# Kernel tuning notes

Hardware: AMD Instinct MI355X
Metric: run time of the kernel (lower is better)

## Reference

```python
import jax, jax.numpy as jnp
import numpy as np

DZ, DB, DS, DX, BATCH, T = 128, 32, 32, 64, 64, 4096


def setup_inputs() -> dict:
    # AW initialized as in PLRNN.init_AW: eye + (1/dz^2) M M^T, spectral norm 1
    rng = np.random.default_rng(0)
    M = rng.standard_normal((DZ, DZ)).astype(np.float32)
    A = np.eye(DZ, dtype=np.float32) + (M @ M.T) / (DZ * DZ)
    A = A / np.max(np.abs(np.linalg.eigvals(A)))
    AW = jnp.asarray(0.95 * A, dtype=jnp.float32)  # 0.95 margin keeps long rollout stable

    key = jax.random.key(0)
    ks = jax.random.split(key, 7)
    z0 = jax.random.normal(ks[0], (BATCH, DZ), dtype=jnp.float32)
    inputs = jax.random.normal(ks[1], (T, DS), dtype=jnp.float32)
    h = 0.1 * jax.random.normal(ks[2], (DZ,), dtype=jnp.float32)
    thetas = 2.0 * jax.random.normal(ks[3], (DZ, DB), dtype=jnp.float32) - 1.0
    alphas = 2.0 * jax.random.normal(ks[4], (DB,), dtype=jnp.float32) - 1.0
    clipping = 5.0 * jnp.ones((DZ, DB), dtype=jnp.float32)  # fixed buffer in torch
    C = 0.1 * jax.random.normal(ks[5], (DZ, DS), dtype=jnp.float32)
    B_obs = jax.random.normal(ks[6], (DZ, DX), dtype=jnp.float32)
    return dict(z0=z0, inputs=inputs, AW=AW, h=h, thetas=thetas,
                alphas=alphas, clipping=clipping, C=C, B_obs=B_obs)


def _leaky(x):
    # nn.LeakyReLU(0.18)
    return jnp.where(x >= 0, x, 0.18 * x)


def reference(z0, inputs, AW, h, thetas, alphas, clipping, C, B_obs):
    # split_diag_offdiag: A = diag(AW), W = AW - diag(AW)
    a_diag = jnp.diag(AW)            # (dz,)
    W = AW - jnp.diag(a_diag)        # (dz, dz), zero diagonal

    def step(z, s):
        # z: (B, dz), s: (ds,)
        d = z[:, :, None] - thetas   # (B, dz, db)
        be = (jnp.sum(alphas * _leaky(d), axis=-1)
              - jnp.sum(alphas * _leaky(d + clipping), axis=-1))  # (B, dz)
        z_new = z * a_diag + be @ W.T + h + (C @ s)  # diag matmul == elementwise
        return z_new, z_new

    _, Z = jax.lax.scan(step, z0, inputs)   # (T, B, dz)
    # torch.cat over list of (B, dz) -> (T*B, dz), time-major
    Z = Z.reshape(-1, Z.shape[-1])
    return Z @ B_obs                        # linear_observation: (T*B, dx)
```

## Files before the change

### kernel.cpp

```cpp
#include <hip/hip_runtime.h>
#include <hip/hip_bf16.h>
#include <hip/hip_fp16.h>

#define DZ 128
#define DB 32
#define DSIN 32
#define DX 64
#define NB 64
#define TT 4096

typedef short v8s __attribute__((ext_vector_type(8)));
typedef float v4f __attribute__((ext_vector_type(4)));
typedef _Float16 v2h __attribute__((ext_vector_type(2)));

__device__ __forceinline__ float dpp_xor1(float x) {
  int y = __builtin_amdgcn_mov_dpp(__builtin_bit_cast(int, x), 0xB1, 0xF, 0xF, true);
  return __builtin_bit_cast(float, y);
}
__device__ __forceinline__ float dpp_xor2(float x) {
  int y = __builtin_amdgcn_mov_dpp(__builtin_bit_cast(int, x), 0x4E, 0xF, 0xF, true);
  return __builtin_bit_cast(float, y);
}

__device__ __forceinline__ short f2bf(float f) {
  __hip_bfloat16 h = __float2bfloat16(f);
  return *reinterpret_cast<short*>(&h);
}

__device__ __forceinline__ unsigned cvt_pk_bf16(float lo, float hi) {
  unsigned r;
  asm volatile("v_cvt_pk_bf16_f32 %0, %1, %2" : "=v"(r) : "v"(lo), "v"(hi));
  return r;
}

__device__ __forceinline__ v2h pk2h(float a, float b) {
  return __builtin_bit_cast(v2h, __builtin_amdgcn_cvt_pkrtz(a, b));
}
__device__ __forceinline__ float fdot2(v2h a, v2h b, float c) {
  return __builtin_amdgcn_fdot2(a, b, c, false);
}

__global__ void k_prep(const float* __restrict__ AW, const float* __restrict__ alphas,
                       const float* __restrict__ clip, float* __restrict__ WCd) {
  __shared__ float cd[DZ];
  int j = threadIdx.x;
  float s = 0.f;
  for (int k = 0; k < DB; ++k) s = fmaf(alphas[k], clip[j * DB + k], s);
  cd[j] = s;
  __syncthreads();
  float acc = 0.f;
  for (int jj = 0; jj < DZ; ++jj)
    if (jj != j) acc = fmaf(AW[j * DZ + jj], cd[jj], acc);
  WCd[j] = acc;
}

__global__ void k_u(const float* __restrict__ inp, const float* __restrict__ h,
                    const float* __restrict__ C, const float* __restrict__ WCd,
                    float* __restrict__ UT) {
  int gid = blockIdx.x * blockDim.x + threadIdx.x;
  int i = gid >> 10;
  int t0 = (gid & 1023) * 4;
  float base = h[i] - WCd[i];
  const float4* c4 = (const float4*)(C + i * DSIN);
  float4 cv[8];
#pragma unroll
  for (int s = 0; s < 8; ++s) cv[s] = c4[s];
  float out[4];
#pragma unroll
  for (int tt = 0; tt < 4; ++tt) {
    const float4* i4 = (const float4*)(inp + (size_t)(t0 + tt) * DSIN);
    float u = base;
#pragma unroll
    for (int s = 0; s < 8; ++s) {
      float4 iv = i4[s];
      u = fmaf(cv[s].x, iv.x, u);
      u = fmaf(cv[s].y, iv.y, u);
      u = fmaf(cv[s].z, iv.z, u);
      u = fmaf(cv[s].w, iv.w, u);
    }
    out[tt] = u;
  }
  *(float4*)(UT + (size_t)i * TT + t0) = make_float4(out[0], out[1], out[2], out[3]);
}

__global__ __launch_bounds__(256, 1) void k_scan(
    const float* __restrict__ z0, const float* __restrict__ AW,
    const float* __restrict__ thetas, const float* __restrict__ alphas,
    const float* __restrict__ clip, const float* __restrict__ UT,
    unsigned* __restrict__ Z32) {
  __shared__ __align__(16) unsigned gpk[2][64];
  const int b = blockIdx.x;
  const int tid = threadIdx.x;
  const int p = tid >> 2, s = tid & 3;
  const int i0 = 2 * p, i1 = i0 + 1;
  const int c0 = 32 * s;

  v2h w0[16], w1[16];
#pragma unroll
  for (int j = 0; j < 16; ++j) {
    float2 a0 = *(const float2*)(AW + (size_t)i0 * DZ + c0 + 2 * j);
    float2 a1 = *(const float2*)(AW + (size_t)i1 * DZ + c0 + 2 * j);
    bool dg = (c0 + 2 * j == i0);
    w0[j] = pk2h(dg ? 0.f : a0.x, a0.y);
    w1[j] = pk2h(a1.x, dg ? 0.f : a1.y);
  }
  const float ad0 = AW[(size_t)i0 * DZ + i0], ad1 = AW[(size_t)i1 * DZ + i1];

  v2h th0[4], th1[4], nc0[4], nc1[4], al[4];
#pragma unroll
  for (int m = 0; m < 4; ++m) {
    int k = 8 * s + 2 * m;
    th0[m] = pk2h(thetas[i0 * DB + k], thetas[i0 * DB + k + 1]);
    th1[m] = pk2h(thetas[i1 * DB + k], thetas[i1 * DB + k + 1]);
    nc0[m] = pk2h(-clip[i0 * DB + k], -clip[i0 * DB + k + 1]);
    nc1[m] = pk2h(-clip[i1 * DB + k], -clip[i1 * DB + k + 1]);
    al[m] = pk2h(-0.82f * alphas[k], -0.82f * alphas[k + 1]);
  }

  float zA = z0[b * DZ + i0], zB = z0[b * DZ + i1];
  const float4* upA = (const float4*)(UT + (size_t)i0 * TT);
  const float4* upB = (const float4*)(UT + (size_t)i1 * TT);
  float4 ugA = upA[0], ugB = upB[0];
  unsigned* zp = Z32 + (size_t)b * 64 + p;
  const v2h zero2 = pk2h(0.f, 0.f);

#pragma unroll 1
  for (int tg = 0; tg < TT / 4; ++tg) {
    int tn = (tg + 1 < TT / 4) ? tg + 1 : tg;
    float4 ugAn = upA[tn], ugBn = upB[tn];
    float uA[4] = {ugA.x, ugA.y, ugA.z, ugA.w};
    float uB[4] = {ugB.x, ugB.y, ugB.z, ugB.w};
#pragma unroll
    for (int q = 0; q < 4; ++q) {
      unsigned* gq = gpk[q & 1];
      v2h zA2 = pk2h(zA, zA), zB2 = pk2h(zB, zB);
      float gA0 = 0.f, gA1 = 0.f, gB0 = 0.f, gB1 = 0.f;
#pragma unroll
      for (int m = 0; m < 4; m += 2) {
        v2h dA0 = __builtin_elementwise_min(
            __builtin_elementwise_max(zA2 - th0[m], nc0[m]), zero2);
        v2h dA1 = __builtin_elementwise_min(
            __builtin_elementwise_max(zA2 - th0[m + 1], nc0[m + 1]), zero2);
        v2h dB0 = __builtin_elementwise_min(
            __builtin_elementwise_max(zB2 - th1[m], nc1[m]), zero2);
        v2h dB1 = __builtin_elementwise_min(
            __builtin_elementwise_max(zB2 - th1[m + 1], nc1[m + 1]), zero2);
        gA0 = fdot2(al[m], dA0, gA0);
        gA1 = fdot2(al[m + 1], dA1, gA1);
        gB0 = fdot2(al[m], dB0, gB0);
        gB1 = fdot2(al[m + 1], dB1, gB1);
      }
      float gA = gA0 + gA1;
      gA += dpp_xor1(gA);
      gA += dpp_xor2(gA);
      float gB = gB0 + gB1;
      gB += dpp_xor1(gB);
      gB += dpp_xor2(gB);
      if (s == 0) gq[p] = __builtin_bit_cast(unsigned, pk2h(gA, gB));
      asm volatile("s_waitcnt lgkmcnt(0)\n\ts_barrier" ::: "memory");

      const uint4* g4 = ((const uint4*)gq) + 4 * s;
      float mA0 = 0.f, mA1 = 0.f, mA2 = 0.f, mA3 = 0.f;
      float mB0 = 0.f, mB1 = 0.f, mB2 = 0.f, mB3 = 0.f;
#pragma unroll
      for (int r = 0; r < 4; ++r) {
        uint4 qd = g4[r];
        v2h q0 = __builtin_bit_cast(v2h, qd.x), q1 = __builtin_bit_cast(v2h, qd.y);
        v2h q2 = __builtin_bit_cast(v2h, qd.z), q3 = __builtin_bit_cast(v2h, qd.w);
        mA0 = fdot2(w0[4 * r + 0], q0, mA0);
        mA1 = fdot2(w0[4 * r + 1], q1, mA1);
        mA2 = fdot2(w0[4 * r + 2], q2, mA2);
        mA3 = fdot2(w0[4 * r + 3], q3, mA3);
        mB0 = fdot2(w1[4 * r + 0], q0, mB0);
        mB1 = fdot2(w1[4 * r + 1], q1, mB1);
        mB2 = fdot2(w1[4 * r + 2], q2, mB2);
        mB3 = fdot2(w1[4 * r + 3], q3, mB3);
      }
      float mA = (mA0 + mA1) + (mA2 + mA3);
      mA += dpp_xor1(mA);
      mA += dpp_xor2(mA);
      float mB = (mB0 + mB1) + (mB2 + mB3);
      mB += dpp_xor1(mB);
      mB += dpp_xor2(mB);
      zA = fmaf(zA, ad0, mA + uA[q]);
      zB = fmaf(zB, ad1, mB + uB[q]);
      if (s == 0) zp[(size_t)(tg * 4 + q) * (NB * 64)] = cvt_pk_bf16(zA, zB);
    }
    ugA = ugAn;
    ugB = ugBn;
  }
}

__global__ __launch_bounds__(256) void k_obs(const short* __restrict__ Z,
                                             const float* __restrict__ Bo,
                                             float* __restrict__ out) {
  const int lane = threadIdx.x & 63;
  const int wv = threadIdx.x >> 6;
  const int rl = lane & 15;
  const int g = lane >> 4;

  v8s bfr[4][4];
#pragma unroll
  for (int nt = 0; nt < 4; ++nt) {
#pragma unroll
    for (int ks = 0; ks < 4; ++ks) {
      v8s f;
#pragma unroll
      for (int m = 0; m < 8; ++m) {
        int k = ks * 32 + g * 8 + m;
        f[m] = f2bf(Bo[k * DX + nt * 16 + rl]);
      }
      bfr[nt][ks] = f;
    }
  }

#pragma unroll
  for (int it = 0; it < 4; ++it) {
    const int r0 = blockIdx.x * 256 + it * 64 + wv * 16;
    const short* zrow = Z + (size_t)(r0 + rl) * DZ;
    v8s afr[4];
#pragma unroll
    for (int ks = 0; ks < 4; ++ks)
      afr[ks] = *(const v8s*)(zrow + ks * 32 + g * 8);
    v4f acc[4];
#pragma unroll
    for (int nt = 0; nt < 4; ++nt) acc[nt] = (v4f){0.f, 0.f, 0.f, 0.f};
#pragma unroll
    for (int nt = 0; nt < 4; ++nt) {
#pragma unroll
      for (int ks = 0; ks < 4; ++ks)
        acc[nt] = __builtin_amdgcn_mfma_f32_16x16x32_bf16(afr[ks], bfr[nt][ks], acc[nt], 0, 0, 0);
    }
#pragma unroll
    for (int nt = 0; nt < 4; ++nt) {
#pragma unroll
      for (int q = 0; q < 4; ++q)
        out[(size_t)(r0 + g * 4 + q) * DX + nt * 16 + rl] = acc[nt][q];
    }
  }
}

extern "C" void kernel_launch(void* const* d_in, const int* in_sizes, int n_in,
                              void* d_out, int out_size, void* d_ws, size_t ws_size,
                              hipStream_t stream) {
  const float* z0 = (const float*)d_in[0];
  const float* inp = (const float*)d_in[1];
  const float* AW = (const float*)d_in[2];
  const float* h = (const float*)d_in[3];
  const float* thetas = (const float*)d_in[4];
  const float* alphas = (const float*)d_in[5];
  const float* clip = (const float*)d_in[6];
  const float* C = (const float*)d_in[7];
  const float* Bo = (const float*)d_in[8];
  float* out = (float*)d_out;

  char* ws = (char*)d_ws;
  float* WCd = (float*)ws;
  float* UT = (float*)(ws + 1024);
  short* Z = (short*)(ws + 1024 + (size_t)TT * DZ * 4);

  k_prep<<<1, 128, 0, stream>>>(AW, alphas, clip, WCd);
  k_u<<<(DZ * TT / 4) / 256, 256, 0, stream>>>(inp, h, C, WCd, UT);
  k_scan<<<NB, 256, 0, stream>>>(z0, AW, thetas, alphas, clip, UT, (unsigned*)Z);
  k_obs<<<(TT * NB) / 256, 256, 0, stream>>>(Z, Bo, out);
}
```

Before: 1.635 ms.

## Process two batch rows per scan block to amortize barriers

The scan kernel now handles two batch elements per workgroup, launching NB/2 blocks instead of NB. Both rows share the same register-resident weights, thresholds and input terms, and one barrier per timestep serves both recurrences, which gives extra independent work to hide latency. The cost is twice the per-step arithmetic on each block's critical path and more register use, while only half as many CUs are occupied.

```diff
diff --git a/kernel.cpp b/kernel.cpp
--- a/kernel.cpp
+++ b/kernel.cpp
@@ -88,8 +88,9 @@
     const float* __restrict__ thetas, const float* __restrict__ alphas,
     const float* __restrict__ clip, const float* __restrict__ UT,
     unsigned* __restrict__ Z32) {
-  __shared__ __align__(16) unsigned gpk[2][64];
-  const int b = blockIdx.x;
+  __shared__ __align__(16) unsigned gpk[2][2][64];
+  const int blk = blockIdx.x;
+  const int b0 = 2 * blk, b1 = b0 + 1;
   const int tid = threadIdx.x;
   const int p = tid >> 2, s = tid & 3;
   const int i0 = 2 * p, i1 = i0 + 1;
@@ -117,11 +118,13 @@
     al[m] = pk2h(-0.82f * alphas[k], -0.82f * alphas[k + 1]);
   }
 
-  float zA = z0[b * DZ + i0], zB = z0[b * DZ + i1];
+  float zA0 = z0[b0 * DZ + i0], zB0 = z0[b0 * DZ + i1];
+  float zA1 = z0[b1 * DZ + i0], zB1 = z0[b1 * DZ + i1];
   const float4* upA = (const float4*)(UT + (size_t)i0 * TT);
   const float4* upB = (const float4*)(UT + (size_t)i1 * TT);
   float4 ugA = upA[0], ugB = upB[0];
-  unsigned* zp = Z32 + (size_t)b * 64 + p;
+  unsigned* zp0 = Z32 + (size_t)b0 * 64 + p;
+  unsigned* zp1 = Z32 + (size_t)b1 * 64 + p;
   const v2h zero2 = pk2h(0.f, 0.f);
 
 #pragma unroll 1
@@ -132,59 +135,122 @@
     float uB[4] = {ugB.x, ugB.y, ugB.z, ugB.w};
 #pragma unroll
     for (int q = 0; q < 4; ++q) {
-      unsigned* gq = gpk[q & 1];
-      v2h zA2 = pk2h(zA, zA), zB2 = pk2h(zB, zB);
-      float gA0 = 0.f, gA1 = 0.f, gB0 = 0.f, gB1 = 0.f;
+      unsigned(*gq)[64] = gpk[q & 1];
+      v2h zA20 = pk2h(zA0, zA0), zB20 = pk2h(zB0, zB0);
+      float gA0a = 0.f, gA0b = 0.f, gB0a = 0.f, gB0b = 0.f;
 #pragma unroll
       for (int m = 0; m < 4; m += 2) {
         v2h dA0 = __builtin_elementwise_min(
-            __builtin_elementwise_max(zA2 - th0[m], nc0[m]), zero2);
+            __builtin_elementwise_max(zA20 - th0[m], nc0[m]), zero2);
         v2h dA1 = __builtin_elementwise_min(
-            __builtin_elementwise_max(zA2 - th0[m + 1], nc0[m + 1]), zero2);
+            __builtin_elementwise_max(zA20 - th0[m + 1], nc0[m + 1]), zero2);
         v2h dB0 = __builtin_elementwise_min(
-            __builtin_elementwise_max(zB2 - th1[m], nc1[m]), zero2);
+            __builtin_elementwise_max(zB20 - th1[m], nc1[m]), zero2);
         v2h dB1 = __builtin_elementwise_min(
-            __builtin_elementwise_max(zB2 - th1[m + 1], nc1[m + 1]), zero2);
-        gA0 = fdot2(al[m], dA0, gA0);
-        gA1 = fdot2(al[m + 1], dA1, gA1);
-        gB0 = fdot2(al[m], dB0, gB0);
-        gB1 = fdot2(al[m + 1], dB1, gB1);
-      }
-      float gA = gA0 + gA1;
-      gA += dpp_xor1(gA);
-      gA += dpp_xor2(gA);
-      float gB = gB0 + gB1;
-      gB += dpp_xor1(gB);
-      gB += dpp_xor2(gB);
-      if (s == 0) gq[p] = __builtin_bit_cast(unsigned, pk2h(gA, gB));
+            __builtin_elementwise_max(zB20 - th1[m + 1], nc1[m + 1]), zero2);
+        gA0a = fdot2(al[m], dA0, gA0a);
+        gA0b = fdot2(al[m + 1], dA1, gA0b);
+        gB0a = fdot2(al[m], dB0, gB0a);
+        gB0b = fdot2(al[m + 1], dB1, gB0b);
+      }
+      float gA_0 = gA0a + gA0b;
+      gA_0 += dpp_xor1(gA_0);
+      gA_0 += dpp_xor2(gA_0);
+      float gB_0 = gB0a + gB0b;
+      gB_0 += dpp_xor1(gB_0);
+      gB_0 += dpp_xor2(gB_0);
+      if (s == 0) gq[0][p] = __builtin_bit_cast(unsigned, pk2h(gA_0, gB_0));
+      v2h zA21 = pk2h(zA1, zA1), zB21 = pk2h(zB1, zB1);
+      float gA1a = 0.f, gA1b = 0.f, gB1a = 0.f, gB1b = 0.f;
+#pragma unroll
+      for (int m = 0; m < 4; m += 2) {
+        v2h dA0 = __builtin_elementwise_min(
+            __builtin_elementwise_max(zA21 - th0[m], nc0[m]), zero2);
+        v2h dA1 = __builtin_elementwise_min(
+            __builtin_elementwise_max(zA21 - th0[m + 1], nc0[m + 1]), zero2);
+        v2h dB0 = __builtin_elementwise_min(
+            __builtin_elementwise_max(zB21 - th1[m], nc1[m]), zero2);
+        v2h dB1 = __builtin_elementwise_min(
+            __builtin_elementwise_max(zB21 - th1[m + 1], nc1[m + 1]), zero2);
+        gA1a = fdot2(al[m], dA0, gA1a);
+        gA1b = fdot2(al[m + 1], dA1, gA1b);
+        gB1a = fdot2(al[m], dB0, gB1a);
+        gB1b = fdot2(al[m + 1], dB1, gB1b);
+      }
+      float gA_1 = gA1a + gA1b;
+      gA_1 += dpp_xor1(gA_1);
+      gA_1 += dpp_xor2(gA_1);
+      float gB_1 = gB1a + gB1b;
+      gB_1 += dpp_xor1(gB_1);
+      gB_1 += dpp_xor2(gB_1);
+      if (s == 0) gq[1][p] = __builtin_bit_cast(unsigned, pk2h(gA_1, gB_1));
       asm volatile("s_waitcnt lgkmcnt(0)\n\ts_barrier" ::: "memory");
 
-      const uint4* g4 = ((const uint4*)gq) + 4 * s;
-      float mA0 = 0.f, mA1 = 0.f, mA2 = 0.f, mA3 = 0.f;
-      float mB0 = 0.f, mB1 = 0.f, mB2 = 0.f, mB3 = 0.f;
-#pragma unroll
-      for (int r = 0; r < 4; ++r) {
-        uint4 qd = g4[r];
-        v2h q0 = __builtin_bit_cast(v2h, qd.x), q1 = __builtin_bit_cast(v2h, qd.y);
-        v2h q2 = __builtin_bit_cast(v2h, qd.z), q3 = __builtin_bit_cast(v2h, qd.w);
-        mA0 = fdot2(w0[4 * r + 0], q0, mA0);
-        mA1 = fdot2(w0[4 * r + 1], q1, mA1);
-        mA2 = fdot2(w0[4 * r + 2], q2, mA2);
-        mA3 = fdot2(w0[4 * r + 3], q3, mA3);
-        mB0 = fdot2(w1[4 * r + 0], q0, mB0);
-        mB1 = fdot2(w1[4 * r + 1], q1, mB1);
-        mB2 = fdot2(w1[4 * r + 2], q2, mB2);
-        mB3 = fdot2(w1[4 * r + 3], q3, mB3);
-      }
-      float mA = (mA0 + mA1) + (mA2 + mA3);
-      mA += dpp_xor1(mA);
-      mA += dpp_xor2(mA);
-      float mB = (mB0 + mB1) + (mB2 + mB3);
-      mB += dpp_xor1(mB);
-      mB += dpp_xor2(mB);
-      zA = fmaf(zA, ad0, mA + uA[q]);
-      zB = fmaf(zB, ad1, mB + uB[q]);
-      if (s == 0) zp[(size_t)(tg * 4 + q) * (NB * 64)] = cvt_pk_bf16(zA, zB);
+      const uint4* g40 = ((const uint4*)gq[0]) + 4 * s;
+      const uint4* g41 = ((const uint4*)gq[1]) + 4 * s;
+      uint4 qd0[4], qd1[4];
+#pragma unroll
+      for (int r = 0; r < 4; ++r) qd0[r] = g40[r];
+#pragma unroll
+      for (int r = 0; r < 4; ++r) qd1[r] = g41[r];
+
+      {
+        float mA0 = 0.f, mA1 = 0.f, mA2 = 0.f, mA3 = 0.f;
+        float mB0 = 0.f, mB1 = 0.f, mB2 = 0.f, mB3 = 0.f;
+#pragma unroll
+        for (int r = 0; r < 4; ++r) {
+          uint4 qd = qd0[r];
+          v2h q0 = __builtin_bit_cast(v2h, qd.x), q1 = __builtin_bit_cast(v2h, qd.y);
+          v2h q2 = __builtin_bit_cast(v2h, qd.z), q3 = __builtin_bit_cast(v2h, qd.w);
+          mA0 = fdot2(w0[4 * r + 0], q0, mA0);
+          mA1 = fdot2(w0[4 * r + 1], q1, mA1);
+          mA2 = fdot2(w0[4 * r + 2], q2, mA2);
+          mA3 = fdot2(w0[4 * r + 3], q3, mA3);
+          mB0 = fdot2(w1[4 * r + 0], q0, mB0);
+          mB1 = fdot2(w1[4 * r + 1], q1, mB1);
+          mB2 = fdot2(w1[4 * r + 2], q2, mB2);
+          mB3 = fdot2(w1[4 * r + 3], q3, mB3);
+        }
+        float mA = (mA0 + mA1) + (mA2 + mA3);
+        mA += dpp_xor1(mA);
+        mA += dpp_xor2(mA);
+        float mB = (mB0 + mB1) + (mB2 + mB3);
+        mB += dpp_xor1(mB);
+        mB += dpp_xor2(mB);
+        zA0 = fmaf(zA0, ad0, mA + uA[q]);
+        zB0 = fmaf(zB0, ad1, mB + uB[q]);
+      }
+      {
+        float mA0 = 0.f, mA1 = 0.f, mA2 = 0.f, mA3 = 0.f;
+        float mB0 = 0.f, mB1 = 0.f, mB2 = 0.f, mB3 = 0.f;
+#pragma unroll
+        for (int r = 0; r < 4; ++r) {
+          uint4 qd = qd1[r];
+          v2h q0 = __builtin_bit_cast(v2h, qd.x), q1 = __builtin_bit_cast(v2h, qd.y);
+          v2h q2 = __builtin_bit_cast(v2h, qd.z), q3 = __builtin_bit_cast(v2h, qd.w);
+          mA0 = fdot2(w0[4 * r + 0], q0, mA0);
+          mA1 = fdot2(w0[4 * r + 1], q1, mA1);
+          mA2 = fdot2(w0[4 * r + 2], q2, mA2);
+          mA3 = fdot2(w0[4 * r + 3], q3, mA3);
+          mB0 = fdot2(w1[4 * r + 0], q0, mB0);
+          mB1 = fdot2(w1[4 * r + 1], q1, mB1);
+          mB2 = fdot2(w1[4 * r + 2], q2, mB2);
+          mB3 = fdot2(w1[4 * r + 3], q3, mB3);
+        }
+        float mA = (mA0 + mA1) + (mA2 + mA3);
+        mA += dpp_xor1(mA);
+        mA += dpp_xor2(mA);
+        float mB = (mB0 + mB1) + (mB2 + mB3);
+        mB += dpp_xor1(mB);
+        mB += dpp_xor2(mB);
+        zA1 = fmaf(zA1, ad0, mA + uA[q]);
+        zB1 = fmaf(zB1, ad1, mB + uB[q]);
+      }
+      if (s == 0) {
+        size_t ofs = (size_t)(tg * 4 + q) * (NB * 64);
+        zp0[ofs] = cvt_pk_bf16(zA0, zB0);
+        zp1[ofs] = cvt_pk_bf16(zA1, zB1);
+      }
     }
     ugA = ugAn;
     ugB = ugBn;
@@ -261,6 +327,6 @@
 
   k_prep<<<1, 128, 0, stream>>>(AW, alphas, clip, WCd);
   k_u<<<(DZ * TT / 4) / 256, 256, 0, stream>>>(inp, h, C, WCd, UT);
-  k_scan<<<NB, 256, 0, stream>>>(z0, AW, thetas, alphas, clip, UT, (unsigned*)Z);
+  k_scan<<<NB / 2, 256, 0, stream>>>(z0, AW, thetas, alphas, clip, UT, (unsigned*)Z);
   k_obs<<<(TT * NB) / 256, 256, 0, stream>>>(Z, Bo, out);
 }
```

Measured after the change: 2.388 ms. +46.1%, slower.

## Split scan step across eight lanes per row pair with packed-half reductions

Applied to the files above, without the earlier changes.

Doubles the scan block to 512 threads, so each output pair of rows is handled by 8 lanes instead of 4. This halves the per-thread basis-expansion and matvec dot-product chains on the serial per-timestep critical path. Cross-lane reductions now run on packed fp16 pairs, using three DPP steps including a half-row mirror, in place of separate fp32 reductions for each row. The cost is twice as many waves meeting at every per-step barrier, and extra rounding error from accumulating partial sums in fp16.

```diff
diff --git a/kernel.cpp b/kernel.cpp
--- a/kernel.cpp
+++ b/kernel.cpp
@@ -13,13 +13,10 @@
 typedef float v4f __attribute__((ext_vector_type(4)));
 typedef _Float16 v2h __attribute__((ext_vector_type(2)));
 
-__device__ __forceinline__ float dpp_xor1(float x) {
-  int y = __builtin_amdgcn_mov_dpp(__builtin_bit_cast(int, x), 0xB1, 0xF, 0xF, true);
-  return __builtin_bit_cast(float, y);
-}
-__device__ __forceinline__ float dpp_xor2(float x) {
-  int y = __builtin_amdgcn_mov_dpp(__builtin_bit_cast(int, x), 0x4E, 0xF, 0xF, true);
-  return __builtin_bit_cast(float, y);
+template <int CTRL>
+__device__ __forceinline__ v2h dpp_h2(v2h x) {
+  int y = __builtin_amdgcn_mov_dpp(__builtin_bit_cast(int, x), CTRL, 0xF, 0xF, true);
+  return __builtin_bit_cast(v2h, y);
 }
 
 __device__ __forceinline__ short f2bf(float f) {
@@ -83,7 +80,7 @@
   *(float4*)(UT + (size_t)i * TT + t0) = make_float4(out[0], out[1], out[2], out[3]);
 }
 
-__global__ __launch_bounds__(256, 1) void k_scan(
+__global__ __launch_bounds__(512, 1) void k_scan(
     const float* __restrict__ z0, const float* __restrict__ AW,
     const float* __restrict__ thetas, const float* __restrict__ alphas,
     const float* __restrict__ clip, const float* __restrict__ UT,
@@ -91,13 +88,13 @@
   __shared__ __align__(16) unsigned gpk[2][64];
   const int b = blockIdx.x;
   const int tid = threadIdx.x;
-  const int p = tid >> 2, s = tid & 3;
+  const int p = tid >> 3, s = tid & 7;
   const int i0 = 2 * p, i1 = i0 + 1;
-  const int c0 = 32 * s;
-
-  v2h w0[16], w1[16];
-#pragma unroll
-  for (int j = 0; j < 16; ++j) {
+  const int c0 = 16 * s;
+
+  v2h w0[8], w1[8];
+#pragma unroll
+  for (int j = 0; j < 8; ++j) {
     float2 a0 = *(const float2*)(AW + (size_t)i0 * DZ + c0 + 2 * j);
     float2 a1 = *(const float2*)(AW + (size_t)i1 * DZ + c0 + 2 * j);
     bool dg = (c0 + 2 * j == i0);
@@ -106,10 +103,10 @@
   }
   const float ad0 = AW[(size_t)i0 * DZ + i0], ad1 = AW[(size_t)i1 * DZ + i1];
 
-  v2h th0[4], th1[4], nc0[4], nc1[4], al[4];
-#pragma unroll
-  for (int m = 0; m < 4; ++m) {
-    int k = 8 * s + 2 * m;
+  v2h th0[2], th1[2], nc0[2], nc1[2], al[2];
+#pragma unroll
+  for (int m = 0; m < 2; ++m) {
+    int k = 4 * s + 2 * m;
     th0[m] = pk2h(thetas[i0 * DB + k], thetas[i0 * DB + k + 1]);
     th1[m] = pk2h(thetas[i1 * DB + k], thetas[i1 * DB + k + 1]);
     nc0[m] = pk2h(-clip[i0 * DB + k], -clip[i0 * DB + k + 1]);
@@ -134,54 +131,51 @@
     for (int q = 0; q < 4; ++q) {
       unsigned* gq = gpk[q & 1];
       v2h zA2 = pk2h(zA, zA), zB2 = pk2h(zB, zB);
-      float gA0 = 0.f, gA1 = 0.f, gB0 = 0.f, gB1 = 0.f;
-#pragma unroll
-      for (int m = 0; m < 4; m += 2) {
-        v2h dA0 = __builtin_elementwise_min(
+      float gA = 0.f, gB = 0.f;
+#pragma unroll
+      for (int m = 0; m < 2; ++m) {
+        v2h dA = __builtin_elementwise_min(
             __builtin_elementwise_max(zA2 - th0[m], nc0[m]), zero2);
-        v2h dA1 = __builtin_elementwise_min(
-            __builtin_elementwise_max(zA2 - th0[m + 1], nc0[m + 1]), zero2);
-        v2h dB0 = __builtin_elementwise_min(
+        v2h dB = __builtin_elementwise_min(
             __builtin_elementwise_max(zB2 - th1[m], nc1[m]), zero2);
-        v2h dB1 = __builtin_elementwise_min(
-            __builtin_elementwise_max(zB2 - th1[m + 1], nc1[m + 1]), zero2);
-        gA0 = fdot2(al[m], dA0, gA0);
-        gA1 = fdot2(al[m + 1], dA1, gA1);
-        gB0 = fdot2(al[m], dB0, gB0);
-        gB1 = fdot2(al[m + 1], dB1, gB1);
+        gA = fdot2(al[m], dA, gA);
+        gB = fdot2(al[m], dB, gB);
       }
-      float gA = gA0 + gA1;
-      gA += dpp_xor1(gA);
-      gA += dpp_xor2(gA);
-      float gB = gB0 + gB1;
-      gB += dpp_xor1(gB);
-      gB += dpp_xor2(gB);
-      if (s == 0) gq[p] = __builtin_bit_cast(unsigned, pk2h(gA, gB));
+      v2h gp = pk2h(gA, gB);
+      gp = gp + dpp_h2<0xB1>(gp);
+      gp = gp + dpp_h2<0x4E>(gp);
+      gp = gp + dpp_h2<0x141>(gp);
+      if (s == 0) gq[p] = __builtin_bit_cast(unsigned, gp);
       asm volatile("s_waitcnt lgkmcnt(0)\n\ts_barrier" ::: "memory");
 
-      const uint4* g4 = ((const uint4*)gq) + 4 * s;
-      float mA0 = 0.f, mA1 = 0.f, mA2 = 0.f, mA3 = 0.f;
-      float mB0 = 0.f, mB1 = 0.f, mB2 = 0.f, mB3 = 0.f;
-#pragma unroll
-      for (int r = 0; r < 4; ++r) {
-        uint4 qd = g4[r];
-        v2h q0 = __builtin_bit_cast(v2h, qd.x), q1 = __builtin_bit_cast(v2h, qd.y);
-        v2h q2 = __builtin_bit_cast(v2h, qd.z), q3 = __builtin_bit_cast(v2h, qd.w);
-        mA0 = fdot2(w0[4 * r + 0], q0, mA0);
-        mA1 = fdot2(w0[4 * r + 1], q1, mA1);
-        mA2 = fdot2(w0[4 * r + 2], q2, mA2);
-        mA3 = fdot2(w0[4 * r + 3], q3, mA3);
-        mB0 = fdot2(w1[4 * r + 0], q0, mB0);
-        mB1 = fdot2(w1[4 * r + 1], q1, mB1);
-        mB2 = fdot2(w1[4 * r + 2], q2, mB2);
-        mB3 = fdot2(w1[4 * r + 3], q3, mB3);
-      }
-      float mA = (mA0 + mA1) + (mA2 + mA3);
-      mA += dpp_xor1(mA);
-      mA += dpp_xor2(mA);
-      float mB = (mB0 + mB1) + (mB2 + mB3);
-      mB += dpp_xor1(mB);
-      mB += dpp_xor2(mB);
+      const uint4* g4 = ((const uint4*)gq) + 2 * s;
+      uint4 qa = g4[0], qb = g4[1];
+      float mA0 = 0.f, mA1 = 0.f, mB0 = 0.f, mB1 = 0.f;
+      v2h q0 = __builtin_bit_cast(v2h, qa.x), q1 = __builtin_bit_cast(v2h, qa.y);
+      v2h q2 = __builtin_bit_cast(v2h, qa.z), q3 = __builtin_bit_cast(v2h, qa.w);
+      v2h q4 = __builtin_bit_cast(v2h, qb.x), q5 = __builtin_bit_cast(v2h, qb.y);
+      v2h q6 = __builtin_bit_cast(v2h, qb.z), q7 = __builtin_bit_cast(v2h, qb.w);
+      mA0 = fdot2(w0[0], q0, mA0);
+      mA1 = fdot2(w0[1], q1, mA1);
+      mB0 = fdot2(w1[0], q0, mB0);
+      mB1 = fdot2(w1[1], q1, mB1);
+      mA0 = fdot2(w0[2], q2, mA0);
+      mA1 = fdot2(w0[3], q3, mA1);
+      mB0 = fdot2(w1[2], q2, mB0);
+      mB1 = fdot2(w1[3], q3, mB1);
+      mA0 = fdot2(w0[4], q4, mA0);
+      mA1 = fdot2(w0[5], q5, mA1);
+      mB0 = fdot2(w1[4], q4, mB0);
+      mB1 = fdot2(w1[5], q5, mB1);
+      mA0 = fdot2(w0[6], q6, mA0);
+      mA1 = fdot2(w0[7], q7, mA1);
+      mB0 = fdot2(w1[6], q6, mB0);
+      mB1 = fdot2(w1[7], q7, mB1);
+      v2h mp = pk2h(mA0 + mA1, mB0 + mB1);
+      mp = mp + dpp_h2<0xB1>(mp);
+      mp = mp + dpp_h2<0x4E>(mp);
+      mp = mp + dpp_h2<0x141>(mp);
+      float mA = (float)mp.x, mB = (float)mp.y;
       zA = fmaf(zA, ad0, mA + uA[q]);
       zB = fmaf(zB, ad1, mB + uB[q]);
       if (s == 0) zp[(size_t)(tg * 4 + q) * (NB * 64)] = cvt_pk_bf16(zA, zB);
@@ -261,6 +255,6 @@
 
   k_prep<<<1, 128, 0, stream>>>(AW, alphas, clip, WCd);
   k_u<<<(DZ * TT / 4) / 256, 256, 0, stream>>>(inp, h, C, WCd, UT);
-  k_scan<<<NB, 256, 0, stream>>>(z0, AW, thetas, alphas, clip, UT, (unsigned*)Z);
+  k_scan<<<NB, 512, 0, stream>>>(z0, AW, thetas, alphas, clip, UT, (unsigned*)Z);
   k_obs<<<(TT * NB) / 256, 256, 0, stream>>>(Z, Bo, out);
 }
```

Measured after the change: 1.580 ms. 1.03x faster.
